# Optimization experiments

Hardware: AMD Instinct MI355X
Metric: run time of the kernel (lower is better)

## Reference

```python
import jax, jax.numpy as jnp
import numpy as np

N = 50000   # nodes
E = 600000  # edges (avg degree 12)
D = 128     # embedding dim (hardcoded in original: np.zeros(128))
P = 5       # propagation iterations (self.p)


def setup_inputs() -> dict:
    key = jax.random.key(0)
    ks = jax.random.split(key, 10)
    x = jax.random.normal(ks[0], (N, D), jnp.float32)
    g = jax.random.normal(ks[1], (D,), jnp.float32)
    dist = jax.random.uniform(ks[2], (E,), jnp.float32)
    w1 = jax.random.normal(ks[3], (1,), jnp.float32)
    w2 = jax.random.normal(ks[4], (1,), jnp.float32)
    w3 = jax.random.normal(ks[5], (1,), jnp.float32)
    w4 = jax.random.normal(ks[6], (1,), jnp.float32)
    w5 = jax.random.normal(ks[7], (1,), jnp.float32)
    src = jax.random.randint(ks[8], (E,), 0, N)
    dst = jax.random.randint(ks[9], (E,), 0, N)
    return {"x": x, "g": g, "dist": dist, "w1": w1, "w2": w2, "w3": w3,
            "w4": w4, "w5": w5, "src": src, "dst": dst}


def reference(x, g, dist, w1, w2, w3, w4, w5, src, dst):
    # travel_times[i] = sum_{j in N(i)} w5 * dist(i,j)  -- iteration-invariant
    travel = jax.ops.segment_sum(w5[0] * dist, src, num_segments=N)  # [N]
    # per-node affine part, constant across the P iterations
    base = w1[0] * x + w2[0] * g[None, :] + w4[0] * jax.nn.relu(travel)[:, None]  # [N, D]
    u = x  # new_u_vect starts as a copy of x
    for _ in range(P):
        # u_sum[i] = sum_{j in N(i)} u[j]  (gather + segment-sum, synchronous update)
        u_sum = jax.ops.segment_sum(u[dst], src, num_segments=N)  # [N, D]
        u = base + w3[0] * u_sum
    return jax.nn.relu(u)
```

## Files before the change

### kernel.cpp

```cpp
#include <hip/hip_runtime.h>

#define D 128
#define D4 32
#define CAPH 32

typedef float v4f __attribute__((ext_vector_type(4)));
typedef _Float16 h4 __attribute__((ext_vector_type(4)));

static inline size_t align_up(size_t v, size_t a) { return (v + a - 1) & ~(a - 1); }

__global__ void fill_ell_kernel(const int* __restrict__ src,
                                const int* __restrict__ dst,
                                const float* __restrict__ dist,
                                unsigned long long* __restrict__ packedA,
                                unsigned long long* __restrict__ packedB,
                                unsigned short* __restrict__ adjA,
                                unsigned short* __restrict__ adjB,
                                int E, int Ehalf) {
  int e = blockIdx.x * blockDim.x + threadIdx.x;
  if (e >= E) return;
  int s = src[e];
  unsigned long long fx = (unsigned long long)(dist[e] * 4294967296.0f);
  unsigned long long val = (1ull << 48) | fx;
  if (e < Ehalf) {
    unsigned long long old = atomicAdd(&packedA[s], val);
    unsigned int slot = (unsigned int)(old >> 48);
    if (slot < CAPH) adjA[(size_t)s * CAPH + slot] = (unsigned short)dst[e];
  } else {
    unsigned long long old = atomicAdd(&packedB[s], val);
    unsigned int slot = (unsigned int)(old >> 48);
    if (slot < CAPH) adjB[(size_t)s * CAPH + slot] = (unsigned short)dst[e];
  }
}

__global__ void base_seed_kernel(const v4f* __restrict__ x4, const v4f* __restrict__ g4,
                                 const unsigned long long* __restrict__ packedA,
                                 const unsigned long long* __restrict__ packedB,
                                 const float* __restrict__ w1p, const float* __restrict__ w2p,
                                 const float* __restrict__ w4p, const float* __restrict__ w5p,
                                 h4* __restrict__ base, h4* __restrict__ uA,
                                 h4* __restrict__ uB, int n) {
  int i = blockIdx.x * blockDim.x + threadIdx.x;
  int node = i >> 5;
  int lane = i & 31;
  if (node > n) return;
  size_t idx = (size_t)i;
  if (node == n) {
    h4 z = {0, 0, 0, 0};
    uA[idx] = z;
    uB[idx] = z;
    return;
  }
  v4f xv = x4[(size_t)node * D4 + lane];
  v4f gv = g4[lane];
  unsigned long long sum = (packedA[node] & 0xFFFFFFFFFFFFull)
                         + (packedB[node] & 0xFFFFFFFFFFFFull);
  float ds = (float)sum * (1.0f / 4294967296.0f);
  float t = w5p[0] * ds;
  t = t > 0.f ? t : 0.f;
  v4f b = w1p[0] * xv + w2p[0] * gv;
  b += t * w4p[0];
  base[idx] = __builtin_convertvector(b, h4);
  uA[idx] = __builtin_convertvector(xv, h4);
}

__global__ __launch_bounds__(256) void prop_kernel(
    const h4* __restrict__ uin, const h4* __restrict__ base,
    const unsigned long long* __restrict__ packedA,
    const unsigned long long* __restrict__ packedB,
    const unsigned short* __restrict__ adjA,
    const unsigned short* __restrict__ adjB,
    const float* __restrict__ w3p,
    void* __restrict__ uout, int n, int final_relu)
{
  int gtid = blockIdx.x * blockDim.x + threadIdx.x;
  int node = gtid >> 5;
  int lane = gtid & 31;
  if (node >= n) return;

  unsigned long long pA = packedA[node];
  unsigned long long pB = packedB[node];
  int degA = (int)(pA >> 48); if (degA > CAPH) degA = CAPH;
  int degB = (int)(pB >> 48); if (degB > CAPH) degB = CAPH;

  int a0 = adjA[(size_t)node * CAPH + lane];
  int a1 = adjB[(size_t)node * CAPH + lane];

  v4f acc0 = {0.f,0.f,0.f,0.f}, acc1 = acc0, acc2 = acc0, acc3 = acc0;

  for (int k = 0; k < degA; k += 8) {
    int j0 = __shfl(a0, k + 0, 32); j0 = (k + 0 < degA) ? j0 : n;
    int j1 = __shfl(a0, k + 1, 32); j1 = (k + 1 < degA) ? j1 : n;
    int j2 = __shfl(a0, k + 2, 32); j2 = (k + 2 < degA) ? j2 : n;
    int j3 = __shfl(a0, k + 3, 32); j3 = (k + 3 < degA) ? j3 : n;
    int j4 = __shfl(a0, k + 4, 32); j4 = (k + 4 < degA) ? j4 : n;
    int j5 = __shfl(a0, k + 5, 32); j5 = (k + 5 < degA) ? j5 : n;
    int j6 = __shfl(a0, k + 6, 32); j6 = (k + 6 < degA) ? j6 : n;
    int j7 = __shfl(a0, k + 7, 32); j7 = (k + 7 < degA) ? j7 : n;
    h4 v0 = uin[(size_t)j0 * 32 + lane];
    h4 v1 = uin[(size_t)j1 * 32 + lane];
    h4 v2 = uin[(size_t)j2 * 32 + lane];
    h4 v3 = uin[(size_t)j3 * 32 + lane];
    h4 v4 = uin[(size_t)j4 * 32 + lane];
    h4 v5 = uin[(size_t)j5 * 32 + lane];
    h4 v6 = uin[(size_t)j6 * 32 + lane];
    h4 v7 = uin[(size_t)j7 * 32 + lane];
    acc0 += __builtin_convertvector(v0, v4f) + __builtin_convertvector(v1, v4f);
    acc1 += __builtin_convertvector(v2, v4f) + __builtin_convertvector(v3, v4f);
    acc2 += __builtin_convertvector(v4, v4f) + __builtin_convertvector(v5, v4f);
    acc3 += __builtin_convertvector(v6, v4f) + __builtin_convertvector(v7, v4f);
  }
  for (int k = 0; k < degB; k += 8) {
    int j0 = __shfl(a1, k + 0, 32); j0 = (k + 0 < degB) ? j0 : n;
    int j1 = __shfl(a1, k + 1, 32); j1 = (k + 1 < degB) ? j1 : n;
    int j2 = __shfl(a1, k + 2, 32); j2 = (k + 2 < degB) ? j2 : n;
    int j3 = __shfl(a1, k + 3, 32); j3 = (k + 3 < degB) ? j3 : n;
    int j4 = __shfl(a1, k + 4, 32); j4 = (k + 4 < degB) ? j4 : n;
    int j5 = __shfl(a1, k + 5, 32); j5 = (k + 5 < degB) ? j5 : n;
    int j6 = __shfl(a1, k + 6, 32); j6 = (k + 6 < degB) ? j6 : n;
    int j7 = __shfl(a1, k + 7, 32); j7 = (k + 7 < degB) ? j7 : n;
    h4 v0 = uin[(size_t)j0 * 32 + lane];
    h4 v1 = uin[(size_t)j1 * 32 + lane];
    h4 v2 = uin[(size_t)j2 * 32 + lane];
    h4 v3 = uin[(size_t)j3 * 32 + lane];
    h4 v4 = uin[(size_t)j4 * 32 + lane];
    h4 v5 = uin[(size_t)j5 * 32 + lane];
    h4 v6 = uin[(size_t)j6 * 32 + lane];
    h4 v7 = uin[(size_t)j7 * 32 + lane];
    acc0 += __builtin_convertvector(v0, v4f) + __builtin_convertvector(v1, v4f);
    acc1 += __builtin_convertvector(v2, v4f) + __builtin_convertvector(v3, v4f);
    acc2 += __builtin_convertvector(v4, v4f) + __builtin_convertvector(v5, v4f);
    acc3 += __builtin_convertvector(v6, v4f) + __builtin_convertvector(v7, v4f);
  }
  v4f asum = (acc0 + acc1) + (acc2 + acc3);

  size_t idx = (size_t)gtid - (size_t)0;
  idx = (size_t)node * 32 + lane;
  v4f bb = __builtin_convertvector(base[idx], v4f);
  v4f r = bb + w3p[0] * asum;

  if (final_relu) {
    r.x = r.x > 0.f ? r.x : 0.f;
    r.y = r.y > 0.f ? r.y : 0.f;
    r.z = r.z > 0.f ? r.z : 0.f;
    r.w = r.w > 0.f ? r.w : 0.f;
    __builtin_nontemporal_store(r, (v4f*)uout + idx);
  } else {
    ((h4*)uout)[idx] = __builtin_convertvector(r, h4);
  }
}

extern "C" void kernel_launch(void* const* d_in, const int* in_sizes, int n_in,
                              void* d_out, int out_size, void* d_ws, size_t ws_size,
                              hipStream_t stream) {
  const float* x    = (const float*)d_in[0];
  const float* g    = (const float*)d_in[1];
  const float* dist = (const float*)d_in[2];
  const float* w1   = (const float*)d_in[3];
  const float* w2   = (const float*)d_in[4];
  const float* w3   = (const float*)d_in[5];
  const float* w4   = (const float*)d_in[6];
  const float* w5   = (const float*)d_in[7];
  const int*   src  = (const int*)d_in[8];
  const int*   dst  = (const int*)d_in[9];

  const int N = in_sizes[0] / D;
  const int E = in_sizes[2];
  const int Ehalf = E / 2;

  char* ws = (char*)d_ws;
  size_t o = 0;
  unsigned long long* packedA = (unsigned long long*)(ws + o); o += align_up((size_t)N * 8, 256);
  unsigned long long* packedB = (unsigned long long*)(ws + o);
  size_t zero_end = o + (size_t)N * 8;
  o += align_up((size_t)N * 8, 256);
  unsigned short* adjA = (unsigned short*)(ws + o); o += align_up((size_t)N * CAPH * 2, 256);
  unsigned short* adjB = (unsigned short*)(ws + o); o += align_up((size_t)N * CAPH * 2, 256);
  h4* baseB = (h4*)(ws + o); o += align_up((size_t)(N + 1) * D * 2, 256);
  h4* uA    = (h4*)(ws + o); o += align_up((size_t)(N + 1) * D * 2, 256);
  h4* uB    = (h4*)(ws + o); o += align_up((size_t)(N + 1) * D * 2, 256);
  float* out = (float*)d_out;

  hipMemsetAsync(ws, 0, zero_end, stream);

  const int tb = 256;
  const int eblocks = (E + tb - 1) / tb;
  const int sthreads = (N + 1) * 32;
  const int sblocks = (sthreads + tb - 1) / tb;

  fill_ell_kernel<<<eblocks, tb, 0, stream>>>(src, dst, dist, packedA, packedB,
                                              adjA, adjB, E, Ehalf);
  base_seed_kernel<<<sblocks, tb, 0, stream>>>((const v4f*)x, (const v4f*)g,
                                               packedA, packedB,
                                               w1, w2, w4, w5, baseB, uA, uB, N);

  const int pthreads = N * 32;
  const int pblocks = (pthreads + 255) / 256;
  prop_kernel<<<pblocks, 256, 0, stream>>>(uA, baseB, packedA, packedB, adjA, adjB, w3, uB,  N, 0);
  prop_kernel<<<pblocks, 256, 0, stream>>>(uB, baseB, packedA, packedB, adjA, adjB, w3, uA,  N, 0);
  prop_kernel<<<pblocks, 256, 0, stream>>>(uA, baseB, packedA, packedB, adjA, adjB, w3, uB,  N, 0);
  prop_kernel<<<pblocks, 256, 0, stream>>>(uB, baseB, packedA, packedB, adjA, adjB, w3, uA,  N, 0);
  prop_kernel<<<pblocks, 256, 0, stream>>>(uA, baseB, packedA, packedB, adjA, adjB, w3, out, N, 1);
}
```

Baseline: 253.2 us.

## Split feature dimension across paired blocks with 16-lane node groups in propagation

```diff
diff --git a/kernel.cpp b/kernel.cpp
--- a/kernel.cpp
+++ b/kernel.cpp
@@ -73,9 +73,11 @@
     const float* __restrict__ w3p,
     void* __restrict__ uout, int n, int final_relu)
 {
-  int gtid = blockIdx.x * blockDim.x + threadIdx.x;
-  int node = gtid >> 5;
-  int lane = gtid & 31;
+  int half  = blockIdx.x & 1;
+  int chunk = blockIdx.x >> 1;
+  int group = threadIdx.x >> 4;
+  int lane  = threadIdx.x & 15;
+  int node  = chunk * 16 + group;
   if (node >= n) return;
 
   unsigned long long pA = packedA[node];
@@ -83,50 +85,58 @@
   int degA = (int)(pA >> 48); if (degA > CAPH) degA = CAPH;
   int degB = (int)(pB >> 48); if (degB > CAPH) degB = CAPH;
 
-  int a0 = adjA[(size_t)node * CAPH + lane];
-  int a1 = adjB[(size_t)node * CAPH + lane];
+  const unsigned short* rowA = adjA + (size_t)node * CAPH;
+  const unsigned short* rowB = adjB + (size_t)node * CAPH;
+  int a0 = rowA[lane];
+  int a1 = rowA[lane + 16];
+  int b0 = rowB[lane];
+  int b1 = rowB[lane + 16];
+
+  const h4* uh = uin + (size_t)half * 16 + lane;
 
   v4f acc0 = {0.f,0.f,0.f,0.f}, acc1 = acc0, acc2 = acc0, acc3 = acc0;
 
   for (int k = 0; k < degA; k += 8) {
-    int j0 = __shfl(a0, k + 0, 32); j0 = (k + 0 < degA) ? j0 : n;
-    int j1 = __shfl(a0, k + 1, 32); j1 = (k + 1 < degA) ? j1 : n;
-    int j2 = __shfl(a0, k + 2, 32); j2 = (k + 2 < degA) ? j2 : n;
-    int j3 = __shfl(a0, k + 3, 32); j3 = (k + 3 < degA) ? j3 : n;
-    int j4 = __shfl(a0, k + 4, 32); j4 = (k + 4 < degA) ? j4 : n;
-    int j5 = __shfl(a0, k + 5, 32); j5 = (k + 5 < degA) ? j5 : n;
-    int j6 = __shfl(a0, k + 6, 32); j6 = (k + 6 < degA) ? j6 : n;
-    int j7 = __shfl(a0, k + 7, 32); j7 = (k + 7 < degA) ? j7 : n;
-    h4 v0 = uin[(size_t)j0 * 32 + lane];
-    h4 v1 = uin[(size_t)j1 * 32 + lane];
-    h4 v2 = uin[(size_t)j2 * 32 + lane];
-    h4 v3 = uin[(size_t)j3 * 32 + lane];
-    h4 v4 = uin[(size_t)j4 * 32 + lane];
-    h4 v5 = uin[(size_t)j5 * 32 + lane];
-    h4 v6 = uin[(size_t)j6 * 32 + lane];
-    h4 v7 = uin[(size_t)j7 * 32 + lane];
+    int sel = (k >= 16) ? a1 : a0;
+    int j0 = __shfl(sel, (k + 0) & 15, 16); j0 = (k + 0 < degA) ? j0 : n;
+    int j1 = __shfl(sel, (k + 1) & 15, 16); j1 = (k + 1 < degA) ? j1 : n;
+    int j2 = __shfl(sel, (k + 2) & 15, 16); j2 = (k + 2 < degA) ? j2 : n;
+    int j3 = __shfl(sel, (k + 3) & 15, 16); j3 = (k + 3 < degA) ? j3 : n;
+    int j4 = __shfl(sel, (k + 4) & 15, 16); j4 = (k + 4 < degA) ? j4 : n;
+    int j5 = __shfl(sel, (k + 5) & 15, 16); j5 = (k + 5 < degA) ? j5 : n;
+    int j6 = __shfl(sel, (k + 6) & 15, 16); j6 = (k + 6 < degA) ? j6 : n;
+    int j7 = __shfl(sel, (k + 7) & 15, 16); j7 = (k + 7 < degA) ? j7 : n;
+    h4 v0 = uh[(size_t)j0 * 32];
+    h4 v1 = uh[(size_t)j1 * 32];
+    h4 v2 = uh[(size_t)j2 * 32];
+    h4 v3 = uh[(size_t)j3 * 32];
+    h4 v4 = uh[(size_t)j4 * 32];
+    h4 v5 = uh[(size_t)j5 * 32];
+    h4 v6 = uh[(size_t)j6 * 32];
+    h4 v7 = uh[(size_t)j7 * 32];
     acc0 += __builtin_convertvector(v0, v4f) + __builtin_convertvector(v1, v4f);
     acc1 += __builtin_convertvector(v2, v4f) + __builtin_convertvector(v3, v4f);
     acc2 += __builtin_convertvector(v4, v4f) + __builtin_convertvector(v5, v4f);
     acc3 += __builtin_convertvector(v6, v4f) + __builtin_convertvector(v7, v4f);
   }
   for (int k = 0; k < degB; k += 8) {
-    int j0 = __shfl(a1, k + 0, 32); j0 = (k + 0 < degB) ? j0 : n;
-    int j1 = __shfl(a1, k + 1, 32); j1 = (k + 1 < degB) ? j1 : n;
-    int j2 = __shfl(a1, k + 2, 32); j2 = (k + 2 < degB) ? j2 : n;
-    int j3 = __shfl(a1, k + 3, 32); j3 = (k + 3 < degB) ? j3 : n;
-    int j4 = __shfl(a1, k + 4, 32); j4 = (k + 4 < degB) ? j4 : n;
-    int j5 = __shfl(a1, k + 5, 32); j5 = (k + 5 < degB) ? j5 : n;
-    int j6 = __shfl(a1, k + 6, 32); j6 = (k + 6 < degB) ? j6 : n;
-    int j7 = __shfl(a1, k + 7, 32); j7 = (k + 7 < degB) ? j7 : n;
-    h4 v0 = uin[(size_t)j0 * 32 + lane];
-    h4 v1 = uin[(size_t)j1 * 32 + lane];
-    h4 v2 = uin[(size_t)j2 * 32 + lane];
-    h4 v3 = uin[(size_t)j3 * 32 + lane];
-    h4 v4 = uin[(size_t)j4 * 32 + lane];
-    h4 v5 = uin[(size_t)j5 * 32 + lane];
-    h4 v6 = uin[(size_t)j6 * 32 + lane];
-    h4 v7 = uin[(size_t)j7 * 32 + lane];
+    int sel = (k >= 16) ? b1 : b0;
+    int j0 = __shfl(sel, (k + 0) & 15, 16); j0 = (k + 0 < degB) ? j0 : n;
+    int j1 = __shfl(sel, (k + 1) & 15, 16); j1 = (k + 1 < degB) ? j1 : n;
+    int j2 = __shfl(sel, (k + 2) & 15, 16); j2 = (k + 2 < degB) ? j2 : n;
+    int j3 = __shfl(sel, (k + 3) & 15, 16); j3 = (k + 3 < degB) ? j3 : n;
+    int j4 = __shfl(sel, (k + 4) & 15, 16); j4 = (k + 4 < degB) ? j4 : n;
+    int j5 = __shfl(sel, (k + 5) & 15, 16); j5 = (k + 5 < degB) ? j5 : n;
+    int j6 = __shfl(sel, (k + 6) & 15, 16); j6 = (k + 6 < degB) ? j6 : n;
+    int j7 = __shfl(sel, (k + 7) & 15, 16); j7 = (k + 7 < degB) ? j7 : n;
+    h4 v0 = uh[(size_t)j0 * 32];
+    h4 v1 = uh[(size_t)j1 * 32];
+    h4 v2 = uh[(size_t)j2 * 32];
+    h4 v3 = uh[(size_t)j3 * 32];
+    h4 v4 = uh[(size_t)j4 * 32];
+    h4 v5 = uh[(size_t)j5 * 32];
+    h4 v6 = uh[(size_t)j6 * 32];
+    h4 v7 = uh[(size_t)j7 * 32];
     acc0 += __builtin_convertvector(v0, v4f) + __builtin_convertvector(v1, v4f);
     acc1 += __builtin_convertvector(v2, v4f) + __builtin_convertvector(v3, v4f);
     acc2 += __builtin_convertvector(v4, v4f) + __builtin_convertvector(v5, v4f);
@@ -134,8 +144,7 @@
   }
   v4f asum = (acc0 + acc1) + (acc2 + acc3);
 
-  size_t idx = (size_t)gtid - (size_t)0;
-  idx = (size_t)node * 32 + lane;
+  size_t idx = (size_t)node * 32 + half * 16 + lane;
   v4f bb = __builtin_convertvector(base[idx], v4f);
   v4f r = bb + w3p[0] * asum;
 
@@ -194,8 +203,8 @@
                                                packedA, packedB,
                                                w1, w2, w4, w5, baseB, uA, uB, N);
 
-  const int pthreads = N * 32;
-  const int pblocks = (pthreads + 255) / 256;
+  const int chunks = (N + 15) / 16;
+  const int pblocks = chunks * 2;
   prop_kernel<<<pblocks, 256, 0, stream>>>(uA, baseB, packedA, packedB, adjA, adjB, w3, uB,  N, 0);
   prop_kernel<<<pblocks, 256, 0, stream>>>(uB, baseB, packedA, packedB, adjA, adjB, w3, uA,  N, 0);
   prop_kernel<<<pblocks, 256, 0, stream>>>(uA, baseB, packedA, packedB, adjA, adjB, w3, uB,  N, 0);
```

Result: no change. 251.8 us (-0.6%).
